# Performance work log

Hardware: AMD Instinct MI355X
Metric: run time of the kernel (lower is better)

## Reference

```python
import jax, jax.numpy as jnp
import numpy as np

A = 9
H = 384
W = 384
MIN_SIZE = 2.0
NMS_THRESH = 0.7
PRE_NMS = 6000
POST_NMS = 300


def _make_anchors():
    # anchors.generate_anchors((H, W), box_sizes): per-cell (x1, y1, w, h) boxes in
    # feature-map coordinates, one box per (anchor, y, x).
    sizes = []
    for s in (4.0, 8.0, 16.0):
        for r in (0.5, 1.0, 2.0):
            sizes.append((s * np.sqrt(r), s / np.sqrt(r)))
    ys, xs = np.meshgrid(np.arange(H, dtype=np.float32), np.arange(W, dtype=np.float32), indexing='ij')
    cx, cy = xs + 0.5, ys + 0.5
    anch = np.stack([
        np.stack([cx - w / 2, cy - h / 2, np.full_like(cx, w), np.full_like(cx, h)], axis=-1)
        for (w, h) in sizes
    ], axis=0)  # [A, H, W, 4]
    return jnp.asarray(anch, jnp.float32)


def setup_inputs() -> dict:
    key = jax.random.key(0)
    k1, k2 = jax.random.split(key)
    scores = jax.random.uniform(k1, (1, A, H, W), dtype=jnp.float32)
    bbox_deltas = jax.random.normal(k2, (1, 4 * A, H, W), dtype=jnp.float32)
    return {
        'scores': scores,
        'bbox_deltas': bbox_deltas,
        'anchor_boxes': _make_anchors(),
        'image_metadata': jnp.zeros((1, 3), jnp.float32),
    }


def _clip_boxes(boxes, length, width):
    # clip_boxes_batch: clamp everything to >=0, convert (x,y,w,h)->(x1,y1,x2,y2),
    # clip to feature-map bounds, convert back.
    b = jnp.maximum(boxes, 0.0)
    x1, y1, w, h = b[..., 0], b[..., 1], b[..., 2], b[..., 3]
    x2 = x1 + w - 1.0
    y2 = y1 + h - 1.0
    x1 = jnp.minimum(x1, length - 1.0)
    y1 = jnp.minimum(y1, width - 1.0)
    x2 = jnp.minimum(x2, length - 1.0)
    y2 = jnp.minimum(y2, width - 1.0)
    return jnp.stack([x1, y1, x2 - x1 + 1.0, y2 - y1 + 1.0], axis=-1)


def _nms(boxes, valid):
    # Faithful port of the source's sequential NMS: repeatedly pick the remaining
    # box with the largest y2, suppress boxes whose intersection / own-area >= thresh.
    x1, y1, w, h = boxes[:, 0], boxes[:, 1], boxes[:, 2], boxes[:, 3]
    x2 = x1 + w - 1.0
    y2 = y1 + h - 1.0
    areas = w * h
    NEG = jnp.float32(-1e30)

    def cond(st):
        v, keep, cnt = st
        return (cnt < POST_NMS) & jnp.any(v)

    def body(st):
        v, keep, cnt = st
        ind = jnp.argmax(jnp.where(v, y2, NEG))
        xx1 = jnp.maximum(x1, x1[ind])
        yy1 = jnp.maximum(y1, y1[ind])
        xx2 = jnp.minimum(x2, x2[ind])
        yy2 = jnp.minimum(y2, y2[ind])
        inter = jnp.maximum(xx2 - xx1 + 1.0, 0.0) * jnp.maximum(yy2 - yy1 + 1.0, 0.0)
        ratio = inter / areas  # intersection over each candidate's own area (as in source)
        nv = v & (ratio < NMS_THRESH)
        nv = nv.at[ind].set(False)
        return nv, keep.at[cnt].set(ind.astype(jnp.int32)), cnt + 1

    keep0 = jnp.full((POST_NMS,), -1, jnp.int32)
    _, keep, cnt = jax.lax.while_loop(cond, body, (valid, keep0, jnp.int32(0)))
    return keep, cnt


def reference(scores, bbox_deltas, anchor_boxes, image_metadata):
    B = 1
    _, _, Hh, Ww = scores.shape
    # two contiguous .view()s compose to a single reshape
    deltas = bbox_deltas.reshape(B, A, Hh, Ww, 4)
    boxes = anchor_boxes[None] + deltas               # [1, A, H, W, 4]
    clipped = _clip_boxes(boxes, float(Hh), float(Ww))
    keep = (clipped[..., 2] >= MIN_SIZE) & (clipped[..., 3] >= MIN_SIZE)

    N = A * Hh * Ww
    boxes_f = clipped.reshape(N, 4)
    scores_f = scores.reshape(N)
    masked = jnp.where(keep.reshape(N), scores_f, jnp.float32(-jnp.inf))

    # descending score sort, PRE_NMS_TOP_N truncation
    order = jnp.argsort(-masked)[:PRE_NMS]
    props = boxes_f[order]                            # [PRE_NMS, 4]
    sc = masked[order]
    valid = jnp.isfinite(sc)

    keep_idx, cnt = _nms(props, valid)
    sel = props[jnp.maximum(keep_idx, 0)]             # [POST_NMS, 4]
    slot_valid = jnp.arange(POST_NMS) < cnt
    out = jnp.where(slot_valid[:, None], sel, 0.0)[None]  # [1, POST_NMS, 4]
    return out
```

## Files before the change

kernel.cpp:

```cpp
#include <hip/hip_runtime.h>
#include <stdint.h>

#define NN 1327104
#define NQ 331776
#define NB 1296
#define PRE_NMS_ 6000
#define POST_NMS_ 300
#define LB_CAP 16384
#define NPAD 6144
#define NWORD 96
#define KB 16
#define MATB 192
#define NREP 8


static __device__ __forceinline__ uint32_t score_key(float s) {
  uint32_t b = __float_as_uint(s);
  uint32_t u = b ^ (((int32_t)b < 0) ? 0xFFFFFFFFu : 0x80000000u);
  return ~u;
}

static __device__ __forceinline__ uint32_t f2s(float v) {
  uint32_t b = __float_as_uint(v);
  return b ^ (((int32_t)b < 0) ? 0xFFFFFFFFu : 0x80000000u);
}

static __device__ __forceinline__ void compute_box(float4 an, float4 de,
    float& x1, float& y1, float& wc, float& hc, bool& keep) {
  float bx = fmaxf(an.x + de.x, 0.0f);
  float by = fmaxf(an.y + de.y, 0.0f);
  float bw = fmaxf(an.z + de.z, 0.0f);
  float bh = fmaxf(an.w + de.w, 0.0f);
  float x2 = bx + bw - 1.0f;
  float y2 = by + bh - 1.0f;
  x1 = fminf(bx, 383.0f);
  y1 = fminf(by, 383.0f);
  x2 = fminf(x2, 383.0f);
  y2 = fminf(y2, 383.0f);
  wc = x2 - x1 + 1.0f;
  hc = y2 - y1 + 1.0f;
  keep = (wc >= 2.0f) && (hc >= 2.0f);
}

static __device__ __forceinline__ uint32_t kb18_of(float s) {
  return (uint32_t)(s * 262144.0f);
}

static __device__ __forceinline__ uint32_t wscan(uint32_t v, int l) {
  #pragma unroll
  for (int off = 1; off < 64; off <<= 1) {
    uint32_t u = __shfl_up(v, off);
    if (l >= off) v += u;
  }
  return v;
}

static __device__ __forceinline__ void pick1_f(const uint32_t* __restrict__ h1r,
                                               uint32_t& selR8, uint32_t& base1) {
  int l = threadIdx.x & 63;
  uint32_t a0 = 0, a1 = 0, a2 = 0, a3 = 0, a4 = 0;
  #pragma unroll
  for (int r = 0; r < NREP; ++r) {
    const uint32_t* h1 = h1r + r * 320;
    a0 += h1[l*5]; a1 += h1[l*5+1]; a2 += h1[l*5+2]; a3 += h1[l*5+3]; a4 += h1[l*5+4];
  }
  uint32_t c0 = a0, c1 = c0+a1, c2 = c1+a2, c3 = c2+a3, c4 = c3+a4;
  uint32_t inc = wscan(c4, l);
  uint32_t excl = inc - c4;
  bool hit = (excl < PRE_NMS_) && (inc >= PRE_NMS_);
  unsigned long long hb = __ballot(hit);
  int hl = __ffsll(hb) - 1;
  uint32_t k, cb;
  if      (excl + c0 >= PRE_NMS_) { k = 0; cb = 0;  }
  else if (excl + c1 >= PRE_NMS_) { k = 1; cb = c0; }
  else if (excl + c2 >= PRE_NMS_) { k = 2; cb = c1; }
  else if (excl + c3 >= PRE_NMS_) { k = 3; cb = c2; }
  else                            { k = 4; cb = c3; }
  selR8 = __shfl(l*5u + k, hl);
  base1 = __shfl(excl + cb, hl);
}

static __device__ __forceinline__ void pickT_lds(const uint32_t* __restrict__ h2,
                                                 uint32_t T,
                                                 uint32_t& sel10, uint32_t& base) {
  int l = threadIdx.x & 63;
  uint32_t h[16];
  #pragma unroll
  for (int k = 0; k < 16; ++k) h[k] = h2[l*16 + k];
  uint32_t cum[16]; cum[0] = h[0];
  #pragma unroll
  for (int k = 1; k < 16; ++k) cum[k] = cum[k-1] + h[k];
  uint32_t inc = wscan(cum[15], l);
  uint32_t excl = inc - cum[15];
  bool hit = (excl < T) && (inc >= T);
  unsigned long long hb = __ballot(hit);
  int hl = __ffsll(hb) - 1;
  uint32_t k = 15, cb = cum[14];
  #pragma unroll
  for (int kk = 15; kk >= 0; --kk)
    if (excl + cum[kk] >= T) { k = (uint32_t)kk; cb = kk ? cum[kk-1] : 0u; }
  sel10 = __shfl(l*16u + k, hl);
  base  = __shfl(excl + cb, hl);
}

static __device__ __forceinline__ void emit_item(uint32_t pos, uint32_t d, uint32_t idx,
    const float4* __restrict__ deltas, const float4* __restrict__ anchors,
    uint64_t* __restrict__ keyhi, uint32_t* __restrict__ keylo,
    float4* __restrict__ box4u) {
  float x1, y1, wc, hc; bool keep;
  compute_box(anchors[idx], deltas[idx], x1, y1, wc, hc, keep);
  float y2 = y1 + hc - 1.0f;
  keyhi[pos] = ((uint64_t)f2s(y2) << 32) | (uint32_t)(~d);
  keylo[pos] = ~idx;
  box4u[pos] = make_float4(x1, y1, wc, hc);
}

__global__ __launch_bounds__(256) void k_hA(const float* __restrict__ scores,
                                            const float4* __restrict__ deltas,
                                            const float4* __restrict__ anchors,
                                            uint32_t* __restrict__ darr,
                                            uint32_t* __restrict__ hist1r,
                                            uint32_t* __restrict__ zctr) {
  __shared__ uint32_t lh[320];
  int t = threadIdx.x;
  for (int j = t; j < 320; j += 256) lh[j] = 0;
  __syncthreads();
  int base = blockIdx.x * 256 + t;
  #pragma unroll
  for (int it = 0; it < 4; ++it) {
    int i = base + it * NQ;
    float x1, y1, wc, hc; bool keep;
    compute_box(anchors[i], deltas[i], x1, y1, wc, hc, keep);
    float s = scores[i];
    uint32_t d = keep ? score_key(s) : 0xFF800000u;
    darr[i] = d;
    uint32_t r8 = keep ? (255u - (kb18_of(s) >> 10)) : 256u;
    atomicAdd(&lh[r8], 1u);
  }
  __syncthreads();
  uint32_t* hdst = hist1r + (blockIdx.x & (NREP - 1)) * 320;
  for (int j = t; j < 320; j += 256) {
    uint32_t c = lh[j];
    if (c) atomicAdd(&hdst[j], c);
  }
  if (blockIdx.x == 0) for (int j = t; j < 320; j += 256) zctr[j] = 0;
}

__global__ __launch_bounds__(256) void k_gather(const uint4* __restrict__ dv,
                                                const uint32_t* __restrict__ hist1r,
                                                uint32_t* __restrict__ ctr,
                                                uint64_t* __restrict__ Lb,
                                                uint64_t* __restrict__ keyhi,
                                                uint32_t* __restrict__ keylo,
                                                float4* __restrict__ box4u,
                                                const float4* __restrict__ deltas,
                                                const float4* __restrict__ anchors) {
  __shared__ uint64_t stA[1024];
  __shared__ uint64_t stB[1024];
  __shared__ uint32_t nA, nB, baseA, baseB, s_sel8;
  int t = threadIdx.x;
  if (t < 64) {
    uint32_t sel8, base1;
    pick1_f(hist1r, sel8, base1);
    if (t == 0) { s_sel8 = sel8; nA = 0; nB = 0; }
  }
  if (t == 0 && blockDim.x > 64) {}
  __syncthreads();
  uint32_t selR8 = s_sel8;

  int g = blockIdx.x * 256 + t;
  uint4 v = dv[g];
  uint32_t arr[4] = {v.x, v.y, v.z, v.w};
  #pragma unroll
  for (int k = 0; k < 4; ++k) {
    uint32_t d = arr[k];
    uint32_t idx = (uint32_t)(g * 4 + k);
    uint32_t r8 = (d <= 0x7FFFFFFFu)
                ? (255u - (kb18_of(__uint_as_float(0x7FFFFFFFu - d)) >> 10)) : 256u;
    if (r8 < selR8) {
      uint32_t p = atomicAdd(&nA, 1u);
      stA[p] = ((uint64_t)d << 32) | idx;
    } else if (r8 == selR8) {
      uint32_t q = atomicAdd(&nB, 1u);
      stB[q] = ((uint64_t)d << 32) | idx;
    }
  }
  __syncthreads();
  if (t == 0) {
    baseA = nA ? atomicAdd(&ctr[0], nA)  : 0u;
    baseB = nB ? atomicAdd(&ctr[32], nB) : 0u;
  }
  __syncthreads();
  uint32_t mA = nA, mB = nB, bA = baseA, bB = baseB;
  for (uint32_t j = t; j < mA; j += 256) {
    uint64_t kj = stA[j];
    uint32_t p = bA + j;
    if (p < PRE_NMS_)
      emit_item(p, (uint32_t)(kj >> 32), (uint32_t)kj, deltas, anchors,
                keyhi, keylo, box4u);
  }
  for (uint32_t j = t; j < mB; j += 256) {
    uint32_t q = bB + j;
    if (q < LB_CAP) Lb[q] = stB[j];
  }
}

__global__ __launch_bounds__(256) void k_finish(const uint32_t* __restrict__ ctr,
                                                const uint64_t* __restrict__ Lb,
                                                uint64_t* __restrict__ keyhi,
                                                uint32_t* __restrict__ keylo,
                                                float4* __restrict__ box4u,
                                                const float4* __restrict__ deltas,
                                                const float4* __restrict__ anchors) {
  __shared__ uint32_t lh2[1024];
  __shared__ uint64_t bnd[256];
  __shared__ uint32_t bcnt, lcnt, s_sel10, s_base;
  int t = threadIdx.x;
  for (int j = t; j < 1024; j += 256) lh2[j] = 0;
  if (t == 0) { bcnt = 0; lcnt = 0; }
  __syncthreads();

  uint32_t C1 = ctr[0]; if (C1 > PRE_NMS_) C1 = PRE_NMS_;
  uint32_t Cb = ctr[32]; if (Cb > LB_CAP) Cb = LB_CAP;
  uint32_t T = PRE_NMS_ - C1;

  for (uint32_t j = t; j < Cb; j += 256) {
    uint32_t d = (uint32_t)(Lb[j] >> 32);
    uint32_t r10 = (d <= 0x7FFFFFFFu)
                 ? (1023u - (kb18_of(__uint_as_float(0x7FFFFFFFu - d)) & 1023u)) : 0u;
    atomicAdd(&lh2[r10], 1u);
  }
  __syncthreads();
  if (t < 64) {
    uint32_t sel10 = 0xFFFFFFFFu, b2 = 0;
    if (T > 0) pickT_lds(lh2, T, sel10, b2);
    if (t == 0) { s_sel10 = sel10; s_base = b2; }
  }
  __syncthreads();
  uint32_t sel10 = s_sel10, C2base = s_base;

  for (uint32_t j = t; j < Cb; j += 256) {
    uint64_t kj = Lb[j];
    uint32_t d = (uint32_t)(kj >> 32), idx = (uint32_t)kj;
    uint32_t r10 = (d <= 0x7FFFFFFFu)
                 ? (1023u - (kb18_of(__uint_as_float(0x7FFFFFFFu - d)) & 1023u)) : 0u;
    if (r10 < sel10) {
      uint32_t p = C1 + atomicAdd(&lcnt, 1u);
      if (p < PRE_NMS_) emit_item(p, d, idx, deltas, anchors, keyhi, keylo, box4u);
    } else if (r10 == sel10) {
      uint32_t q = atomicAdd(&bcnt, 1u);
      if (q < 256) bnd[q] = kj;
    }
  }
  __syncthreads();
  uint32_t B = (bcnt < 256u) ? bcnt : 256u;
  uint32_t T2 = (T > C2base) ? (T - C2base) : 0u;
  for (uint32_t j = t; j < B; j += 256) {
    uint64_t kj = bnd[j];
    uint32_t r = 0;
    for (uint32_t k = 0; k < B; ++k) r += (bnd[k] < kj) ? 1u : 0u;
    if (r < T2)
      emit_item(C1 + C2base + r, (uint32_t)(kj >> 32), (uint32_t)kj,
                deltas, anchors, keyhi, keylo, box4u);
  }
  for (int j = PRE_NMS_ + t; j < NPAD; j += 256) {
    keyhi[j] = 0;
    keylo[j] = (uint32_t)(NPAD - j);
    box4u[j] = make_float4(0.f, 0.f, 0.f, 0.f);
  }
}

__global__ __launch_bounds__(512) void k_rank(const uint64_t* __restrict__ keyhi,
                                              const uint32_t* __restrict__ keylo,
                                              uint32_t* __restrict__ rank2d) {
  __shared__ uint64_t shi[768];
  __shared__ uint32_t slo[768];
  int t = threadIdx.x;
  int ib = blockIdx.x >> 3, c = blockIdx.x & 7, base = c * 768;
  for (int j = t; j < 768; j += 512) { shi[j] = keyhi[base + j]; slo[j] = keylo[base + j]; }
  __syncthreads();
  int i = ib * 256 + (t >> 1);
  int h = t & 1;
  uint64_t hi = keyhi[i]; uint32_t lo = keylo[i];
  uint32_t cnt = 0;
  int j0 = h * 384;
  for (int j = j0; j < j0 + 384; ++j) {
    uint64_t hj = shi[j]; uint32_t lj = slo[j];
    cnt += ((hj > hi) || (hj == hi && lj > lo)) ? 1u : 0u;
  }
  rank2d[i * 16 + c * 2 + h] = cnt;
}

__global__ __launch_bounds__(512) void k_matsc(const uint64_t* __restrict__ keyhi,
                                               const uint32_t* __restrict__ rank2d,
                                               const float4* __restrict__ box4u,
                                               float4* __restrict__ sobox,
                                               unsigned long long* __restrict__ valid,
                                               uint64_t* __restrict__ M) {
  __shared__ float4 sb[NPAD];
  __shared__ float  sa[NPAD];
  int t = threadIdx.x;
  int b = blockIdx.x;
  for (int i = t; i < NPAD; i += 512) {
    const uint4* rp = (const uint4*)(rank2d + (size_t)i * 16);
    uint4 r0 = rp[0], r1 = rp[1], r2 = rp[2], r3 = rp[3];
    uint32_t r = r0.x+r0.y+r0.z+r0.w + r1.x+r1.y+r1.z+r1.w
               + r2.x+r2.y+r2.z+r2.w + r3.x+r3.y+r3.z+r3.w;
    float4 bx = box4u[i];
    float x2 = bx.x + bx.z - 1.0f;
    float y2 = bx.y + bx.w - 1.0f;
    sb[r] = make_float4(bx.x, bx.y, x2, y2);
    sa[r] = bx.z * bx.w;
    if (b == 0) {
      sobox[r] = bx;
      uint32_t d = ~(uint32_t)(keyhi[i] & 0xFFFFFFFFu);
      if (d < 0xFF800000u)
        atomicOr(&valid[r >> 6], 1ull << (r & 63));
    }
  }
  __syncthreads();
  int wid = t >> 6, l = t & 63;
  #pragma unroll
  for (int rr = 0; rr < 4; ++rr) {
    int r = b * 32 + wid * 4 + rr;
    float4 rb = sb[r];
    for (int w = 0; w < NWORD; ++w) {
      int j = w * 64 + l;
      float4 cb = sb[j];
      float ca = sa[j];
      float xx1 = fmaxf(cb.x, rb.x), yy1 = fmaxf(cb.y, rb.y);
      float xx2 = fminf(cb.z, rb.z), yy2 = fminf(cb.w, rb.w);
      float iw = fmaxf(xx2 - xx1 + 1.0f, 0.0f);
      float ih = fmaxf(yy2 - yy1 + 1.0f, 0.0f);
      float ratio = (iw * ih) / ca;
      unsigned long long mm = __ballot(!(ratio < 0.7f));
      if (l == 0) M[(size_t)r * NWORD + w] = mm;
    }
  }
}

__global__ __launch_bounds__(1024) void k_seq(const unsigned long long* __restrict__ valid,
                                              const uint64_t* __restrict__ M,
                                              const float4* __restrict__ sobox,
                                              float* __restrict__ out) {
  int t = threadIdx.x;
  if (t >= 64) {
    const uint4* p = (const uint4*)M;
    uint4 acc = make_uint4(0, 0, 0, 0);
    for (int j = t - 64; j < 3072 * 48; j += 960) {
      uint4 v = p[j];
      acc.x ^= v.x; acc.y ^= v.y; acc.z ^= v.z; acc.w ^= v.w;
    }
    asm volatile("" :: "v"(acc.x), "v"(acc.y), "v"(acc.z), "v"(acc.w));
    return;
  }
  __builtin_amdgcn_s_setprio(1);
  int l = t;
  unsigned long long v0 = valid[l];
  unsigned long long v1 = (l < 32) ? valid[64 + l] : 0ull;
  uint32_t cnt = 0;

  for (;;) {
    if (cnt >= POST_NMS_) break;
    unsigned long long B0 = __ballot(v0 != 0ull);
    unsigned long long B1 = __ballot((l < 32) && (v1 != 0ull));
    if ((B0 | B1) == 0ull) break;

    uint64_t p0 = 0, p1 = 0, p2 = 0, p3 = 0;
    int m = 0;
    while (m < KB && (B0 | B1)) {
      int wsel; unsigned long long wv;
      if (B0) { wsel = __ffsll(B0) - 1; B0 &= B0 - 1; wv = __shfl(v0, wsel); }
      else    { int q = __ffsll(B1) - 1; wsel = 64 + q; B1 &= B1 - 1; wv = __shfl(v1, q); }
      while (wv && m < KB) {
        int bb = __ffsll(wv) - 1; wv &= wv - 1;
        uint64_t ins = (uint64_t)(uint32_t)(wsel * 64 + bb) << ((m & 3) * 16);
        if (m < 4) p0 |= ins; else if (m < 8) p1 |= ins;
        else if (m < 12) p2 |= ins; else p3 |= ins;
        ++m;
      }
    }
#define SLOT(k) ((uint32_t)((((k) < 4 ? p0 : (k) < 8 ? p1 : (k) < 12 ? p2 : p3) \
                             >> (((k) & 3) * 16)) & 0xFFFFu))
#define FOR16(F) F(0) F(1) F(2) F(3) F(4) F(5) F(6) F(7) \
                 F(8) F(9) F(10) F(11) F(12) F(13) F(14) F(15)

#define ROWDECL(k) uint64_t rm0_##k = 0, rm1_##k = 0;
    FOR16(ROWDECL)
#undef ROWDECL
#define ROWLOAD(k) if (k < m) { const uint64_t* rp = M + (size_t)SLOT(k) * NWORD; \
                     rm0_##k = rp[l]; rm1_##k = (l < 32) ? rp[64 + l] : 0ull; }
    FOR16(ROWLOAD)
#undef ROWLOAD
    uint64_t pkl = (l < 4) ? p0 : (l < 8) ? p1 : (l < 12) ? p2 : p3;
    uint32_t cj = (uint32_t)((pkl >> ((l & 3) * 16)) & 0xFFFFu);
    float4 obox = make_float4(0.f, 0.f, 0.f, 0.f);
    if (l < KB) obox = sobox[cj];

    uint32_t wj = cj >> 6, bj = cj & 63;
    int srcA = (int)(wj & 63), srcB = (int)(wj & 31);
    uint32_t srow[KB];
#define SROW(k) { uint64_t a = __shfl((unsigned long long)rm0_##k, srcA); \
                  uint64_t b = __shfl((unsigned long long)rm1_##k, srcB); \
                  uint64_t sel = (wj < 64) ? a : b; \
                  uint32_t bit = (l < KB && k < m) ? (uint32_t)((sel >> bj) & 1) : 0u; \
                  srow[k] = (uint32_t)(__ballot(bit) & 0xFFFFull); }
    FOR16(SROW)
#undef SROW

    uint32_t cnt0 = cnt;
    uint32_t wm = 0, supp = 0;
    #pragma unroll
    for (int k = 0; k < KB; ++k) {
      if (k < m && cnt < POST_NMS_ && !((supp >> k) & 1)) {
        wm |= 1u << k; ++cnt; supp |= srow[k];
      }
    }

    if (l < KB && ((wm >> l) & 1)) {
      uint32_t pos = cnt0 + (uint32_t)__popc(wm & ((1u << l) - 1));
      *(float4*)(out + (size_t)pos * 4) = obox;
    }

    uint64_t comb0 = 0, comb1 = 0;
#define COMB(k) if ((wm >> k) & 1) { comb0 |= rm0_##k; comb1 |= rm1_##k; }
    FOR16(COMB)
#undef COMB
#undef FOR16
#undef SLOT
    v0 &= ~comb0; v1 &= ~comb1;
  }
  __builtin_amdgcn_s_setprio(0);

  for (int j = l; j < (int)(POST_NMS_ - cnt) * 4; j += 64) out[cnt * 4 + j] = 0.0f;
}

extern "C" void kernel_launch(void* const* d_in, const int* in_sizes, int n_in,
                              void* d_out, int out_size, void* d_ws, size_t ws_size,
                              hipStream_t stream) {
  const float*  scores  = (const float*)d_in[0];
  const float4* deltas  = (const float4*)d_in[1];
  const float4* anchors = (const float4*)d_in[2];
  float* out = (float*)d_out;

  uint8_t* w8 = (uint8_t*)d_ws;
  uint32_t* darr  = (uint32_t*)w8;
  uint64_t* M     = (uint64_t*)w8;
  float4*   sobox = (float4*)(w8 + 4841472);
  uint64_t* keyhi  = (uint64_t*)(w8 + 5308416);
  uint32_t* keylo  = (uint32_t*)(w8 + 5357568);
  float4*   box4u  = (float4*)  (w8 + 5382144);
  uint32_t* rank2d = (uint32_t*)(w8 + 5480448);
  uint32_t* hist1r = (uint32_t*)(w8 + 5873664);
  uint32_t* ctr    = (uint32_t*)(w8 + 5883904);
  unsigned long long* valid = (unsigned long long*)(w8 + 5884160);
  uint64_t* Lb     = (uint64_t*)(w8 + 5885184);

  const uint4* dv = (const uint4*)darr;

  hipMemsetAsync(hist1r, 0, 10240, stream);

  k_hA    <<<NB, 256, 0, stream>>>(scores, deltas, anchors, darr, hist1r, ctr);
  k_gather<<<NB, 256, 0, stream>>>(dv, hist1r, ctr, Lb, keyhi, keylo, box4u,
                                   deltas, anchors);
  k_finish<<<1, 256, 0, stream>>>(ctr, Lb, keyhi, keylo, box4u, deltas, anchors);
  k_rank  <<<MATB, 512, 0, stream>>>(keyhi, keylo, rank2d);
  k_matsc <<<MATB, 512, 0, stream>>>(keyhi, rank2d, box4u, sobox, valid, M);
  k_seq   <<<1, 1024, 0, stream>>>(valid, M, sobox, out);
}
```

Baseline: 269.6 us.

## Rework sequential NMS candidate batching with scan-based slot fill and column loads

The single-wave greedy NMS loop now picks candidates with a prefix scan over per-word popcounts, writing candidate indices into shared memory, instead of a serial ffs walk over ballots. The candidate batch grows from 16 to 24, and each lane loads its own column bits from the mask matrix directly rather than extracting them through shuffles and ballots. The block shrinks from 1024 to 512 threads, which also halves the helper threads that stream the matrix into cache. The intent is a shorter serial critical path per batch and fewer loop iterations, at the cost of more live registers, extra global loads per batch and a per-step ballot in the greedy loop.

```diff
diff --git a/kernel.cpp b/kernel.cpp
--- a/kernel.cpp
+++ b/kernel.cpp
@@ -9,7 +9,7 @@
 #define LB_CAP 16384
 #define NPAD 6144
 #define NWORD 96
-#define KB 16
+#define KB 24
 #define MATB 192
 #define NREP 8
 
@@ -164,7 +164,6 @@
     pick1_f(hist1r, sel8, base1);
     if (t == 0) { s_sel8 = sel8; nA = 0; nB = 0; }
   }
-  if (t == 0 && blockDim.x > 64) {}
   __syncthreads();
   uint32_t selR8 = s_sel8;
 
@@ -339,15 +338,20 @@
   }
 }
 
-__global__ __launch_bounds__(1024) void k_seq(const unsigned long long* __restrict__ valid,
-                                              const uint64_t* __restrict__ M,
-                                              const float4* __restrict__ sobox,
-                                              float* __restrict__ out) {
+#define FOR24(F) F(0) F(1) F(2) F(3) F(4) F(5) F(6) F(7) \
+                 F(8) F(9) F(10) F(11) F(12) F(13) F(14) F(15) \
+                 F(16) F(17) F(18) F(19) F(20) F(21) F(22) F(23)
+
+__global__ __launch_bounds__(512) void k_seq(const unsigned long long* __restrict__ valid,
+                                             const uint64_t* __restrict__ M,
+                                             const float4* __restrict__ sobox,
+                                             float* __restrict__ out) {
+  __shared__ int cslot[KB];
   int t = threadIdx.x;
   if (t >= 64) {
     const uint4* p = (const uint4*)M;
     uint4 acc = make_uint4(0, 0, 0, 0);
-    for (int j = t - 64; j < 3072 * 48; j += 960) {
+    for (int j = t - 64; j < 3072 * 48; j += 448) {
       uint4 v = p[j];
       acc.x ^= v.x; acc.y ^= v.y; acc.z ^= v.z; acc.w ^= v.w;
     }
@@ -362,60 +366,61 @@
 
   for (;;) {
     if (cnt >= POST_NMS_) break;
-    unsigned long long B0 = __ballot(v0 != 0ull);
-    unsigned long long B1 = __ballot((l < 32) && (v1 != 0ull));
-    if ((B0 | B1) == 0ull) break;
-
-    uint64_t p0 = 0, p1 = 0, p2 = 0, p3 = 0;
-    int m = 0;
-    while (m < KB && (B0 | B1)) {
-      int wsel; unsigned long long wv;
-      if (B0) { wsel = __ffsll(B0) - 1; B0 &= B0 - 1; wv = __shfl(v0, wsel); }
-      else    { int q = __ffsll(B1) - 1; wsel = 64 + q; B1 &= B1 - 1; wv = __shfl(v1, q); }
-      while (wv && m < KB) {
-        int bb = __ffsll(wv) - 1; wv &= wv - 1;
-        uint64_t ins = (uint64_t)(uint32_t)(wsel * 64 + bb) << ((m & 3) * 16);
-        if (m < 4) p0 |= ins; else if (m < 8) p1 |= ins;
-        else if (m < 12) p2 |= ins; else p3 |= ins;
-        ++m;
-      }
-    }
-#define SLOT(k) ((uint32_t)((((k) < 4 ? p0 : (k) < 8 ? p1 : (k) < 12 ? p2 : p3) \
-                             >> (((k) & 3) * 16)) & 0xFFFFu))
-#define FOR16(F) F(0) F(1) F(2) F(3) F(4) F(5) F(6) F(7) \
-                 F(8) F(9) F(10) F(11) F(12) F(13) F(14) F(15)
+    uint32_t n0 = (uint32_t)__popcll(v0);
+    uint32_t inc0 = wscan(n0, l);
+    uint32_t T0 = __shfl(inc0, 63);
+    uint32_t ex0 = inc0 - n0;
+    uint32_t n1 = (uint32_t)__popcll(v1);
+    uint32_t inc1 = wscan(n1, l);
+    uint32_t T1 = __shfl(inc1, 63);
+    uint32_t ex1 = T0 + inc1 - n1;
+    uint32_t TV = T0 + T1;
+    if (TV == 0) break;
+    uint32_t m = (TV < KB) ? TV : KB;
+
+    if (l < KB) cslot[l] = 0;
+    __builtin_amdgcn_sched_barrier(0);
+    if (ex0 < KB) {
+      unsigned long long w = v0; uint32_t r = ex0;
+      while (w && r < KB) { int b = __ffsll(w) - 1; cslot[r] = l * 64 + b; ++r; w &= w - 1; }
+    }
+    if (ex1 < KB && v1) {
+      unsigned long long w = v1; uint32_t r = ex1;
+      while (w && r < KB) { int b = __ffsll(w) - 1; cslot[r] = (64 + l) * 64 + b; ++r; w &= w - 1; }
+    }
+    __builtin_amdgcn_sched_barrier(0);
+
+    int cu0 = cslot[0];
+#define CUDECL(k) int cu_##k = cslot[k];
+    FOR24(CUDECL)
+#undef CUDECL
+    int c_own = (l < KB) ? cslot[l] : cu0;
+    uint32_t ow = (uint32_t)c_own >> 6, ob = (uint32_t)c_own & 63;
 
 #define ROWDECL(k) uint64_t rm0_##k = 0, rm1_##k = 0;
-    FOR16(ROWDECL)
+    FOR24(ROWDECL)
 #undef ROWDECL
-#define ROWLOAD(k) if (k < m) { const uint64_t* rp = M + (size_t)SLOT(k) * NWORD; \
+#define ROWLOAD(k) if (k < (int)m) { const uint64_t* rp = M + (size_t)cu_##k * NWORD; \
                      rm0_##k = rp[l]; rm1_##k = (l < 32) ? rp[64 + l] : 0ull; }
-    FOR16(ROWLOAD)
+    FOR24(ROWLOAD)
 #undef ROWLOAD
-    uint64_t pkl = (l < 4) ? p0 : (l < 8) ? p1 : (l < 12) ? p2 : p3;
-    uint32_t cj = (uint32_t)((pkl >> ((l & 3) * 16)) & 0xFFFFu);
+    uint32_t col = 0;
+#define COLLOAD(k) if (k < (int)m) { \
+                     uint64_t wq = M[(size_t)cu_##k * NWORD + ow]; \
+                     col |= (uint32_t)((wq >> ob) & 1ull) << k; }
+    FOR24(COLLOAD)
+#undef COLLOAD
     float4 obox = make_float4(0.f, 0.f, 0.f, 0.f);
-    if (l < KB) obox = sobox[cj];
-
-    uint32_t wj = cj >> 6, bj = cj & 63;
-    int srcA = (int)(wj & 63), srcB = (int)(wj & 31);
-    uint32_t srow[KB];
-#define SROW(k) { uint64_t a = __shfl((unsigned long long)rm0_##k, srcA); \
-                  uint64_t b = __shfl((unsigned long long)rm1_##k, srcB); \
-                  uint64_t sel = (wj < 64) ? a : b; \
-                  uint32_t bit = (l < KB && k < m) ? (uint32_t)((sel >> bj) & 1) : 0u; \
-                  srow[k] = (uint32_t)(__ballot(bit) & 0xFFFFull); }
-    FOR16(SROW)
-#undef SROW
+    if (l < KB) obox = sobox[c_own];
 
     uint32_t cnt0 = cnt;
-    uint32_t wm = 0, supp = 0;
-    #pragma unroll
-    for (int k = 0; k < KB; ++k) {
-      if (k < m && cnt < POST_NMS_ && !((supp >> k) & 1)) {
-        wm |= 1u << k; ++cnt; supp |= srow[k];
-      }
-    }
+    uint32_t wm = 0;
+#define GREEDY(k) { \
+      unsigned long long bal = __ballot((l == k) && ((col & wm) == 0u)); \
+      if ((k < (int)m) && (cnt < POST_NMS_) && ((bal >> k) & 1ull)) { \
+        wm |= 1u << k; ++cnt; } }
+    FOR24(GREEDY)
+#undef GREEDY
 
     if (l < KB && ((wm >> l) & 1)) {
       uint32_t pos = cnt0 + (uint32_t)__popc(wm & ((1u << l) - 1));
@@ -424,10 +429,8 @@
 
     uint64_t comb0 = 0, comb1 = 0;
 #define COMB(k) if ((wm >> k) & 1) { comb0 |= rm0_##k; comb1 |= rm1_##k; }
-    FOR16(COMB)
+    FOR24(COMB)
 #undef COMB
-#undef FOR16
-#undef SLOT
     v0 &= ~comb0; v1 &= ~comb1;
   }
   __builtin_amdgcn_s_setprio(0);
@@ -466,5 +469,5 @@
   k_finish<<<1, 256, 0, stream>>>(ctr, Lb, keyhi, keylo, box4u, deltas, anchors);
   k_rank  <<<MATB, 512, 0, stream>>>(keyhi, keylo, rank2d);
   k_matsc <<<MATB, 512, 0, stream>>>(keyhi, rank2d, box4u, sobox, valid, M);
-  k_seq   <<<1, 1024, 0, stream>>>(valid, M, sobox, out);
-}
+  k_seq   <<<1, 512, 0, stream>>>(valid, M, sobox, out);
+}
```

Measured after the change: 304.7 us. 1.13x slower.

## Replace serial candidate extraction in NMS loop with wave scan and LDS slots

Applied to the files above, without the earlier changes.

The single-wave NMS loop used to pick up to 16 candidate indices with a serial ballot and find-first-set walk over words. It now prefix-sums the per-lane popcounts with a wave scan and has each lane write its own candidate indices into a small shared array. The extra 15 waves that streamed the suppression matrix to warm the cache are removed, and the launch shrinks to one 64-thread block. In exchange the loop now pays for shared-memory barriers on every iteration and no longer prefetches the matrix into cache.

```diff
diff --git a/kernel.cpp b/kernel.cpp
--- a/kernel.cpp
+++ b/kernel.cpp
@@ -164,7 +164,6 @@
     pick1_f(hist1r, sel8, base1);
     if (t == 0) { s_sel8 = sel8; nA = 0; nB = 0; }
   }
-  if (t == 0 && blockDim.x > 64) {}
   __syncthreads();
   uint32_t selR8 = s_sel8;
 
@@ -339,71 +338,63 @@
   }
 }
 
-__global__ __launch_bounds__(1024) void k_seq(const unsigned long long* __restrict__ valid,
-                                              const uint64_t* __restrict__ M,
-                                              const float4* __restrict__ sobox,
-                                              float* __restrict__ out) {
-  int t = threadIdx.x;
-  if (t >= 64) {
-    const uint4* p = (const uint4*)M;
-    uint4 acc = make_uint4(0, 0, 0, 0);
-    for (int j = t - 64; j < 3072 * 48; j += 960) {
-      uint4 v = p[j];
-      acc.x ^= v.x; acc.y ^= v.y; acc.z ^= v.z; acc.w ^= v.w;
-    }
-    asm volatile("" :: "v"(acc.x), "v"(acc.y), "v"(acc.z), "v"(acc.w));
-    return;
-  }
-  __builtin_amdgcn_s_setprio(1);
-  int l = t;
+#define FOR16(F) F(0) F(1) F(2) F(3) F(4) F(5) F(6) F(7) \
+                 F(8) F(9) F(10) F(11) F(12) F(13) F(14) F(15)
+
+__global__ __launch_bounds__(64) void k_seq(const unsigned long long* __restrict__ valid,
+                                            const uint64_t* __restrict__ M,
+                                            const float4* __restrict__ sobox,
+                                            float* __restrict__ out) {
+  __shared__ int cslot[KB];
+  int l = threadIdx.x;
   unsigned long long v0 = valid[l];
   unsigned long long v1 = (l < 32) ? valid[64 + l] : 0ull;
   uint32_t cnt = 0;
 
   for (;;) {
-    if (cnt >= POST_NMS_) break;
-    unsigned long long B0 = __ballot(v0 != 0ull);
-    unsigned long long B1 = __ballot((l < 32) && (v1 != 0ull));
-    if ((B0 | B1) == 0ull) break;
-
-    uint64_t p0 = 0, p1 = 0, p2 = 0, p3 = 0;
-    int m = 0;
-    while (m < KB && (B0 | B1)) {
-      int wsel; unsigned long long wv;
-      if (B0) { wsel = __ffsll(B0) - 1; B0 &= B0 - 1; wv = __shfl(v0, wsel); }
-      else    { int q = __ffsll(B1) - 1; wsel = 64 + q; B1 &= B1 - 1; wv = __shfl(v1, q); }
-      while (wv && m < KB) {
-        int bb = __ffsll(wv) - 1; wv &= wv - 1;
-        uint64_t ins = (uint64_t)(uint32_t)(wsel * 64 + bb) << ((m & 3) * 16);
-        if (m < 4) p0 |= ins; else if (m < 8) p1 |= ins;
-        else if (m < 12) p2 |= ins; else p3 |= ins;
-        ++m;
-      }
-    }
-#define SLOT(k) ((uint32_t)((((k) < 4 ? p0 : (k) < 8 ? p1 : (k) < 12 ? p2 : p3) \
-                             >> (((k) & 3) * 16)) & 0xFFFFu))
-#define FOR16(F) F(0) F(1) F(2) F(3) F(4) F(5) F(6) F(7) \
-                 F(8) F(9) F(10) F(11) F(12) F(13) F(14) F(15)
+    uint32_t n0 = (uint32_t)__popcll(v0);
+    uint32_t inc0 = wscan(n0, l);
+    uint32_t T0 = __shfl(inc0, 63);
+    uint32_t ex0 = inc0 - n0;
+    uint32_t n1 = (uint32_t)__popcll(v1);
+    uint32_t inc1 = wscan(n1, l);
+    uint32_t T1 = __shfl(inc1, 63);
+    uint32_t ex1 = T0 + inc1 - n1;
+    uint32_t TV = T0 + T1;
+    if (cnt >= POST_NMS_ || TV == 0) break;
+    uint32_t m = (TV < KB) ? TV : KB;
+
+    __syncthreads();
+    if (l < KB) cslot[l] = 0;
+    __syncthreads();
+    if (ex0 < KB) {
+      unsigned long long w = v0; uint32_t r = ex0;
+      while (w && r < KB) { int b = __ffsll(w) - 1; cslot[r] = l * 64 + b; ++r; w &= w - 1; }
+    }
+    if (ex1 < KB && v1) {
+      unsigned long long w = v1; uint32_t r = ex1;
+      while (w && r < KB) { int b = __ffsll(w) - 1; cslot[r] = (64 + l) * 64 + b; ++r; w &= w - 1; }
+    }
+    __syncthreads();
 
 #define ROWDECL(k) uint64_t rm0_##k = 0, rm1_##k = 0;
     FOR16(ROWDECL)
 #undef ROWDECL
-#define ROWLOAD(k) if (k < m) { const uint64_t* rp = M + (size_t)SLOT(k) * NWORD; \
-                     rm0_##k = rp[l]; rm1_##k = (l < 32) ? rp[64 + l] : 0ull; }
+#define ROWLOAD(k) if (k < (int)m) { const uint64_t* p = M + (size_t)cslot[k] * NWORD; \
+                     rm0_##k = p[l]; rm1_##k = (l < 32) ? p[64 + l] : 0ull; }
     FOR16(ROWLOAD)
 #undef ROWLOAD
-    uint64_t pkl = (l < 4) ? p0 : (l < 8) ? p1 : (l < 12) ? p2 : p3;
-    uint32_t cj = (uint32_t)((pkl >> ((l & 3) * 16)) & 0xFFFFu);
     float4 obox = make_float4(0.f, 0.f, 0.f, 0.f);
-    if (l < KB) obox = sobox[cj];
-
+    if (l < KB) obox = sobox[cslot[l]];
+
+    uint32_t cj = (l < KB) ? (uint32_t)cslot[l] : 0u;
     uint32_t wj = cj >> 6, bj = cj & 63;
     int srcA = (int)(wj & 63), srcB = (int)(wj & 31);
     uint32_t srow[KB];
 #define SROW(k) { uint64_t a = __shfl((unsigned long long)rm0_##k, srcA); \
                   uint64_t b = __shfl((unsigned long long)rm1_##k, srcB); \
                   uint64_t sel = (wj < 64) ? a : b; \
-                  uint32_t bit = (l < KB && k < m) ? (uint32_t)((sel >> bj) & 1) : 0u; \
+                  uint32_t bit = (l < KB && k < (int)m) ? (uint32_t)((sel >> bj) & 1) : 0u; \
                   srow[k] = (uint32_t)(__ballot(bit) & 0xFFFFull); }
     FOR16(SROW)
 #undef SROW
@@ -412,7 +403,7 @@
     uint32_t wm = 0, supp = 0;
     #pragma unroll
     for (int k = 0; k < KB; ++k) {
-      if (k < m && cnt < POST_NMS_ && !((supp >> k) & 1)) {
+      if (k < (int)m && cnt < POST_NMS_ && !((supp >> k) & 1)) {
         wm |= 1u << k; ++cnt; supp |= srow[k];
       }
     }
@@ -426,11 +417,8 @@
 #define COMB(k) if ((wm >> k) & 1) { comb0 |= rm0_##k; comb1 |= rm1_##k; }
     FOR16(COMB)
 #undef COMB
-#undef FOR16
-#undef SLOT
     v0 &= ~comb0; v1 &= ~comb1;
   }
-  __builtin_amdgcn_s_setprio(0);
 
   for (int j = l; j < (int)(POST_NMS_ - cnt) * 4; j += 64) out[cnt * 4 + j] = 0.0f;
 }
@@ -466,5 +454,5 @@
   k_finish<<<1, 256, 0, stream>>>(ctr, Lb, keyhi, keylo, box4u, deltas, anchors);
   k_rank  <<<MATB, 512, 0, stream>>>(keyhi, keylo, rank2d);
   k_matsc <<<MATB, 512, 0, stream>>>(keyhi, rank2d, box4u, sobox, valid, M);
-  k_seq   <<<1, 1024, 0, stream>>>(valid, M, sobox, out);
-}
+  k_seq   <<<1, 64, 0, stream>>>(valid, M, sobox, out);
+}
```

After: 255.4 us, median of 2. -5.3%, faster.
